# Kernel tuning notes

Measured on AMD Instinct MI355X. Metric: run time of the kernel, lower is better.

Reference implementation:

```python
import jax, jax.numpy as jnp
import numpy as np

B, H, W = 16, 512, 512


def _nmax(a, pad_val):
    """Max over 3x3 cross (4-neighborhood + center), constant-padded borders."""
    p = jnp.pad(a, ((0, 0), (1, 1), (1, 1)), constant_values=pad_val)
    return jnp.maximum(a, jnp.maximum(
        jnp.maximum(p[:, :-2, 1:-1], p[:, 2:, 1:-1]),
        jnp.maximum(p[:, 1:-1, :-2], p[:, 1:-1, 2:])))


def _dilate(b):
    # cv2 dilate with 3x3 MORPH_ELLIPSE (== cross), border treated as background
    return _nmax(b, 0.0)


def _erode(b):
    # cv2 erode default border value == foreground, so erode = 1 - dilate(1 - b)
    return 1.0 - _nmax(1.0 - b, 0.0)


def setup_inputs() -> dict:
    key = jax.random.key(0)
    x = jax.random.uniform(key, (B, 4, H, W), dtype=jnp.float32)
    return {"x": x}


def reference(x):
    # --- majority vote with disagreement fallback to pred1 ---
    p1 = (x[:, 1] > 0.5).astype(jnp.float32)
    p2 = (x[:, 2] > 0.5).astype(jnp.float32)
    p3 = (x[:, 3] > 0.5).astype(jnp.float32)
    vote = p1 + p2 + p3
    m = jnp.where(vote >= 2, 1.0, jnp.where(vote == 1, p1, 0.0))

    # --- morphology: MORPH_CLOSE then MORPH_OPEN with 3x3 ellipse (cross) ---
    m = _erode(_dilate(m))   # close
    m = _dilate(_erode(m))   # open

    # --- 4-connected CCL (scipy ndimage.label default) via label propagation ---
    Bm, Hm, Wm = m.shape
    mask_i = m > 0
    init = jnp.where(mask_i,
                     jnp.arange(1, Hm * Wm + 1, dtype=jnp.int32).reshape(1, Hm, Wm),
                     jnp.int32(0))

    def cond(s):
        return s[1]

    def body(s):
        lbl, _ = s
        new = jnp.where(mask_i, _nmax(lbl, 0), 0)
        return (new, jnp.any(new != lbl))

    lbl, _ = jax.lax.while_loop(cond, body, (init, jnp.array(True)))

    # --- component sizes and small-component removal ---
    sizes = jax.vmap(lambda mm, ll: jax.ops.segment_sum(
        mm.ravel(), ll.ravel(), num_segments=Hm * Wm + 1))(m, lbl)
    min_size = max(50, int(0.001 * Hm * Wm))  # = 262 for 512x512
    keep = jnp.take_along_axis(sizes, lbl.reshape(Bm, -1), axis=1)
    keep = (keep.reshape(Bm, Hm, Wm) > min_size).astype(jnp.float32)
    m = m * keep
    return m[:, None, :, :]  # [B, 1, H, W]
```

## Files before the change

### kernel.cpp

```cpp
#include <hip/hip_runtime.h>

typedef unsigned long long u64;
typedef unsigned u32;
typedef unsigned char u8;

#define BATCH 16
#define Hh 512
#define Ww 512
#define IMG (Hh * Ww)
#define TOT (BATCH * IMG)
#define WPI 4096
#define WROW 8
#define NWORDS (TOT / 64)
#define MIN_SIZE 262
#define MAXRUNS (NWORDS * 32)

#define BAND 8
#define HALO 4
#define BROWS (BAND + 2 * HALO)
#define BWORDS (BROWS * WROW)
#define MAXBRUNS (64 * 32)
#define NBANDS (BATCH * 64)

__device__ __forceinline__ u32 runstart(u64 bits, int s) {
    u64 ms = (s >= 63) ? ~0ULL : ((1ULL << (s + 1)) - 1);
    u64 nz = ~bits & ms;
    return nz ? (u32)(64 - __clzll(nz)) : 0u;
}
__device__ __forceinline__ u32 runlen(u64 bits, int s) {
    u64 v = ~(bits >> s);
    return v ? (u32)(__ffsll(v) - 1) : (u32)(64 - s);
}
__device__ __forceinline__ u32 runrank(u64 bits, u64 st, int s) {
    u32 rs = runstart(bits, s);
    return (u32)__popcll(st & (((u64)1 << rs) - 1));
}

__device__ __forceinline__ u64 morph_word(const u64* M, int w, int rr, bool er) {
    const u64 B = er ? ~0ULL : 0ULL;
    int wx = w & 7;
    u64 cc = M[w];
    u64 lf = (cc << 1) | (wx > 0 ? (M[w - 1] >> 63) : (er ? 1ULL : 0ULL));
    u64 rt = (cc >> 1) | (wx < 7 ? (M[w + 1] << 63) : (er ? (1ULL << 63) : 0ULL));
    u64 up = (rr <= 0)      ? B : (w >= WROW          ? M[w - WROW] : B);
    u64 dn = (rr >= Hh - 1) ? B : (w < BWORDS - WROW  ? M[w + WROW] : B);
    return er ? (cc & lf & rt & up & dn) : (cc | lf | rt | up | dn);
}

template <typename P>
__device__ __forceinline__ u32 uf_find_halve(P L, u32 x) {
    while (true) {
        u32 p = L[x];
        if (p == x) return x;
        u32 gp = L[p];
        if (gp == p) return p;
        atomicMin(&L[x], gp);
        x = gp;
    }
}
template <typename P>
__device__ __forceinline__ void uf_merge(P L, u32 a, u32 b) {
    while (true) {
        a = uf_find_halve(L, a);
        b = uf_find_halve(L, b);
        if (a == b) return;
        if (a > b) { u32 t = a; a = b; b = t; }
        u32 old = atomicMin(&L[b], a);
        if (old == b) return;
        b = old;
    }
}

__global__ __launch_bounds__(256) void vote_pack_kernel(const float4* __restrict__ x4,
                                                        u64* __restrict__ mp0,
                                                        u32* __restrict__ runCtr) {
    int t = threadIdx.x, blk = blockIdx.x;
    if (blk == 0 && t == 0) *runCtr = 0u;
    int img = blk >> 7;
    size_t p4 = (size_t)(blk & 127) * 512 + (size_t)t * 2;
    const float4* c1 = x4 + ((size_t)img * 4 + 1) * (IMG / 4);
    const float4* c2 = x4 + ((size_t)img * 4 + 2) * (IMG / 4);
    const float4* c3 = x4 + ((size_t)img * 4 + 3) * (IMG / 4);
    u32 m = 0;
    #pragma unroll
    for (int q = 0; q < 2; ++q) {
        float4 a1 = c1[p4 + q], a2 = c2[p4 + q], a3 = c3[p4 + q];
        u32 b0 = (a1.x > 0.5f) | ((a2.x > 0.5f) & (a3.x > 0.5f));
        u32 b1 = (a1.y > 0.5f) | ((a2.y > 0.5f) & (a3.y > 0.5f));
        u32 b2 = (a1.z > 0.5f) | ((a2.z > 0.5f) & (a3.z > 0.5f));
        u32 b3 = (a1.w > 0.5f) | ((a2.w > 0.5f) & (a3.w > 0.5f));
        m |= (b0 | (b1 << 1) | (b2 << 2) | (b3 << 3)) << (q * 4);
    }
    u32 a = m | (__shfl_xor(m, 1) << 8);
    u32 b = a | (__shfl_xor(a, 2) << 16);
    u64 w = (u64)b | ((u64)__shfl_xor(b, 4) << 32);
    if ((t & 7) == 0) mp0[(size_t)blk * 32 + (t >> 3)] = w;
}

__global__ __launch_bounds__(256) void morph_ccl_kernel(const u64* __restrict__ mp0,
                                                        u64* __restrict__ mp,
                                                        u32* __restrict__ L,
                                                        u32* __restrict__ wordbase,
                                                        u32* __restrict__ counts,
                                                        u8*  __restrict__ len8,
                                                        u32* __restrict__ runCtr) {
    __shared__ u64 Ma[BWORDS], Mb[BWORDS];
    __shared__ u32 Ll[MAXBRUNS];
    __shared__ u32 wb_l[64];
    __shared__ u32 baseSh, totSh;
    int blk = blockIdx.x;
    int img = blk >> 6;
    int r0  = (blk & 63) * BAND;
    int t = threadIdx.x;
    int rr = r0 - HALO + (t >> 3);

    if (t < BWORDS)
        Ma[t] = (rr >= 0 && rr < Hh) ? mp0[(size_t)img * WPI + (size_t)rr * WROW + (t & 7)] : 0;
    __syncthreads();

    if (t < BWORDS) Mb[t] = morph_word(Ma, t, rr, false);
    __syncthreads();
    if (t < BWORDS) Ma[t] = morph_word(Mb, t, rr, true);
    __syncthreads();
    if (t < BWORDS) Mb[t] = morph_word(Ma, t, rr, true);
    __syncthreads();
    if (t < BWORDS) Ma[t] = morph_word(Mb, t, rr, false);
    __syncthreads();

    if (t < 64)
        mp[(size_t)img * WPI + (size_t)r0 * WROW + t] = Ma[32 + t];

    u32 myexcl = 0;
    if (t < 64) {
        u64 bits = Ma[32 + t];
        u64 st = bits & ~(bits << 1);
        u32 cnt = __popcll(st);
        u32 inc = cnt;
        #pragma unroll
        for (int d = 1; d < 64; d <<= 1) {
            u32 v = __shfl_up(inc, d);
            if (t >= d) inc += v;
        }
        myexcl = inc - cnt;
        if (t == 63) { baseSh = atomicAdd(runCtr, inc); totSh = inc; }
    }
    __syncthreads();
    u32 base = baseSh, tot = totSh;
    if (t < 64) {
        wb_l[t] = myexcl;
        wordbase[(size_t)img * WPI + (size_t)r0 * WROW + t] = base + myexcl;
    }
    for (u32 i = t; i < tot; i += 256) { Ll[i] = i; counts[base + i] = 0u; }
    __syncthreads();

    if (t < 56) {
        int rp = t >> 3, w = t & 7;
        u64 a = Ma[32 + rp * 8 + w], b = Ma[32 + (rp + 1) * 8 + w];
        u64 ov = a & b, seg = ov & ~(ov << 1);
        if (seg) {
            u64 sta = a & ~(a << 1), stb = b & ~(b << 1);
            u32 ba = wb_l[rp * 8 + w], bb = wb_l[(rp + 1) * 8 + w];
            while (seg) {
                int s = __ffsll(seg) - 1; seg &= seg - 1;
                uf_merge((u32*)Ll, ba + runrank(a, sta, s), bb + runrank(b, stb, s));
            }
        }
    } else if (t >= 64 && t < 120) {
        int ht = t - 64;
        int r = ht / 7, w = 1 + ht % 7;
        u64 a = Ma[32 + r * 8 + w - 1], b = Ma[32 + r * 8 + w];
        if ((a >> 63) & b & 1ULL) {
            u64 sta = a & ~(a << 1);
            uf_merge((u32*)Ll, wb_l[r * 8 + w - 1] + (u32)__popcll(sta & ~(1ULL << 63)) - 1u
                                 + (u32)((sta >> 63) & 1ULL),
                               wb_l[r * 8 + w]);
        }
    }
    __syncthreads();

    if (t < 64) {
        u64 bits = Ma[32 + t];
        u64 st = bits & ~(bits << 1);
        u32 local = wb_l[t];
        while (st) {
            int s = __ffsll(st) - 1; st &= st - 1;
            u32 r = local, p = Ll[r];
            while (p != r) { r = p; p = Ll[r]; }
            L[base + local] = base + r;
            len8[base + local] = (u8)runlen(bits, s);
            local++;
        }
    }
}

#define BITEMS (BATCH * 63 * WROW)
__global__ void border_merge_kernel(const u64* __restrict__ mp,
                                    const u32* __restrict__ wordbase, u32* L) {
    int e = blockIdx.x * blockDim.x + threadIdx.x;
    if (e >= BITEMS) return;
    int w = e & 7, k = (e >> 3) % 63 + 1, img = e / (63 * 8);
    int R = k * BAND;
    size_t wa_i = (size_t)img * WPI + (size_t)(R - 1) * WROW + w;
    size_t wb_i = (size_t)img * WPI + (size_t)R * WROW + w;
    u64 a = mp[wa_i], b = mp[wb_i];
    u64 ov = a & b, seg = ov & ~(ov << 1);
    if (!seg) return;
    u64 sta = a & ~(a << 1), stb = b & ~(b << 1);
    u32 wba = wordbase[wa_i], wbb = wordbase[wb_i];
    while (seg) {
        int s = __ffsll(seg) - 1; seg &= seg - 1;
        uf_merge(L, wba + runrank(a, sta, s), wbb + runrank(b, stb, s));
    }
}

#define ACCUM_STRIDE (1024 * 256)
__global__ __launch_bounds__(256) void accum_kernel(u32* __restrict__ L,
                                                    const u8* __restrict__ len8,
                                                    u32* __restrict__ counts,
                                                    const u32* __restrict__ runCtr) {
    u32 n = *runCtr;
    u32 gid = blockIdx.x * 256 + threadIdx.x;
    int tid = threadIdx.x;
    u32 trips = (n + ACCUM_STRIDE - 1) / ACCUM_STRIDE;
    for (u32 k = 0; k < trips; ++k) {
        u32 id = gid + k * ACCUM_STRIDE;
        bool valid = id < n;
        u32 r = 0xFFFFFFFFu, len = 0;
        if (valid) {
            r = id; u32 p = L[r];
            while (p != r) { r = p; p = L[r]; }
            L[id] = r;
            len = len8[id];
        }
        bool pending = true;
        while (true) {
            u64 act = __ballot(pending);
            if (!act) break;
            int leader = __ffsll(act) - 1;
            u32 lr = __shfl(r, leader);
            bool mine = pending && (r == lr);
            u32 c = mine ? len : 0u;
            c += __shfl_xor(c, 32); c += __shfl_xor(c, 16); c += __shfl_xor(c, 8);
            c += __shfl_xor(c, 4);  c += __shfl_xor(c, 2);  c += __shfl_xor(c, 1);
            if ((tid & 63) == leader && lr != 0xFFFFFFFFu) atomicAdd(&counts[lr], c);
            if (mine) pending = false;
        }
    }
}

__global__ __launch_bounds__(256) void final_kernel(const u64* __restrict__ mp,
                                                    const u32* __restrict__ wordbase,
                                                    const u32* __restrict__ L,
                                                    const u32* __restrict__ counts,
                                                    float* __restrict__ out) {
    __shared__ u64 km[128];
    int tid = threadIdx.x;
    if (tid < 128) {
        int widx = blockIdx.x * 128 + tid;
        u64 bits = mp[widx];
        u64 st = bits & ~(bits << 1);
        u32 id = wordbase[widx];
        u64 keep = 0;
        while (st) {
            int s = __ffsll(st) - 1; st &= st - 1;
            u32 r = L[id++];
            if (counts[r] > MIN_SIZE) {
                u32 len = runlen(bits, s);
                keep |= (len == 64 ? ~0ULL : ((1ULL << len) - 1ULL)) << s;
            }
        }
        km[tid] = keep;
    }
    __syncthreads();
    float4* o4 = (float4*)out + (size_t)blockIdx.x * 2048;
    for (int i = tid; i < 2048; i += 256) {
        u32 nib = (u32)(km[i >> 4] >> ((i & 15) * 4)) & 0xFu;
        o4[i] = make_float4(nib & 1u ? 1.f : 0.f, nib & 2u ? 1.f : 0.f,
                            nib & 4u ? 1.f : 0.f, nib & 8u ? 1.f : 0.f);
    }
}

extern "C" void kernel_launch(void* const* d_in, const int* in_sizes, int n_in,
                              void* d_out, int out_size, void* d_ws, size_t ws_size,
                              hipStream_t stream) {
    const float* x = (const float*)d_in[0];
    float* out = (float*)d_out;

    u64* mp0 = (u64*)d_ws;
    u64* mp  = mp0 + NWORDS;
    u32* wordbase = (u32*)(mp + NWORDS);
    u32* L      = wordbase + NWORDS;
    u32* counts = L + MAXRUNS;
    u8*  len8   = (u8*)(counts + MAXRUNS);
    u32* runCtr = (u32*)(len8 + MAXRUNS);

    const int block = 256;

    vote_pack_kernel<<<2048, block, 0, stream>>>((const float4*)x, mp0, runCtr);
    morph_ccl_kernel<<<NBANDS, block, 0, stream>>>(mp0, mp, L, wordbase, counts, len8, runCtr);
    border_merge_kernel<<<(BITEMS + block - 1) / block, block, 0, stream>>>(mp, wordbase, L);
    accum_kernel<<<1024, block, 0, stream>>>(L, len8, counts, runCtr);
    final_kernel<<<512, block, 0, stream>>>(mp, wordbase, L, counts, out);
}
```

Before: 77.28 us.

## Use fixed per-word run slots and fold border merge into band kernel

Replaces the dynamic run numbering (atomic counter, prefix scan, wordbase and len8 arrays) with fixed 32-slot run IDs per word. The L and counts arrays are now initialised inside the vote/pack kernel. Each band kernel merges its local union-find roots into the global structure and merges its boundary with the next band, which removes the separate border-merge kernel and one launch. The accumulate kernel recomputes run lengths from the bitmask. The trade-off is a sparse label array that must be fully initialised (larger memory writes) and more global atomics issued from the band kernel. The halo also grows by one row, and the local shared array is now indexed by slot rather than by a compact run index.

```diff
diff --git a/kernel.cpp b/kernel.cpp
--- a/kernel.cpp
+++ b/kernel.cpp
@@ -2,7 +2,6 @@
 
 typedef unsigned long long u64;
 typedef unsigned u32;
-typedef unsigned char u8;
 
 #define BATCH 16
 #define Hh 512
@@ -16,10 +15,9 @@
 #define MAXRUNS (NWORDS * 32)
 
 #define BAND 8
-#define HALO 4
+#define HALO 5
 #define BROWS (BAND + 2 * HALO)
 #define BWORDS (BROWS * WROW)
-#define MAXBRUNS (64 * 32)
 #define NBANDS (BATCH * 64)
 
 __device__ __forceinline__ u32 runstart(u64 bits, int s) {
@@ -73,9 +71,13 @@
 
 __global__ __launch_bounds__(256) void vote_pack_kernel(const float4* __restrict__ x4,
                                                         u64* __restrict__ mp0,
-                                                        u32* __restrict__ runCtr) {
+                                                        u32* __restrict__ L,
+                                                        u32* __restrict__ counts) {
     int t = threadIdx.x, blk = blockIdx.x;
-    if (blk == 0 && t == 0) *runCtr = 0u;
+    u32 gidx = (u32)blk * 256 + t;
+    ((uint4*)L)[gidx] = make_uint4(gidx * 4u, gidx * 4u + 1u, gidx * 4u + 2u, gidx * 4u + 3u);
+    ((uint4*)counts)[gidx] = make_uint4(0u, 0u, 0u, 0u);
+
     int img = blk >> 7;
     size_t p4 = (size_t)(blk & 127) * 512 + (size_t)t * 2;
     const float4* c1 = x4 + ((size_t)img * 4 + 1) * (IMG / 4);
@@ -99,15 +101,9 @@
 
 __global__ __launch_bounds__(256) void morph_ccl_kernel(const u64* __restrict__ mp0,
                                                         u64* __restrict__ mp,
-                                                        u32* __restrict__ L,
-                                                        u32* __restrict__ wordbase,
-                                                        u32* __restrict__ counts,
-                                                        u8*  __restrict__ len8,
-                                                        u32* __restrict__ runCtr) {
+                                                        u32* __restrict__ L) {
     __shared__ u64 Ma[BWORDS], Mb[BWORDS];
-    __shared__ u32 Ll[MAXBRUNS];
-    __shared__ u32 wb_l[64];
-    __shared__ u32 baseSh, totSh;
+    __shared__ u32 Ll[2048];
     int blk = blockIdx.x;
     int img = blk >> 6;
     int r0  = (blk & 63) * BAND;
@@ -116,6 +112,7 @@
 
     if (t < BWORDS)
         Ma[t] = (rr >= 0 && rr < Hh) ? mp0[(size_t)img * WPI + (size_t)rr * WROW + (t & 7)] : 0;
+    for (int i = t; i < 2048; i += 256) Ll[i] = (u32)i;
     __syncthreads();
 
     if (t < BWORDS) Mb[t] = morph_word(Ma, t, rr, false);
@@ -127,129 +124,110 @@
     if (t < BWORDS) Ma[t] = morph_word(Mb, t, rr, false);
     __syncthreads();
 
+    const int OWN = HALO * WROW;
+    u32 gwbase = (u32)img * WPI + (u32)r0 * WROW;
     if (t < 64)
-        mp[(size_t)img * WPI + (size_t)r0 * WROW + t] = Ma[32 + t];
-
-    u32 myexcl = 0;
-    if (t < 64) {
-        u64 bits = Ma[32 + t];
-        u64 st = bits & ~(bits << 1);
-        u32 cnt = __popcll(st);
-        u32 inc = cnt;
-        #pragma unroll
-        for (int d = 1; d < 64; d <<= 1) {
-            u32 v = __shfl_up(inc, d);
-            if (t >= d) inc += v;
-        }
-        myexcl = inc - cnt;
-        if (t == 63) { baseSh = atomicAdd(runCtr, inc); totSh = inc; }
-    }
-    __syncthreads();
-    u32 base = baseSh, tot = totSh;
-    if (t < 64) {
-        wb_l[t] = myexcl;
-        wordbase[(size_t)img * WPI + (size_t)r0 * WROW + t] = base + myexcl;
-    }
-    for (u32 i = t; i < tot; i += 256) { Ll[i] = i; counts[base + i] = 0u; }
-    __syncthreads();
+        mp[(size_t)gwbase + t] = Ma[OWN + t];
 
     if (t < 56) {
         int rp = t >> 3, w = t & 7;
-        u64 a = Ma[32 + rp * 8 + w], b = Ma[32 + (rp + 1) * 8 + w];
+        u64 a = Ma[OWN + rp * 8 + w], b = Ma[OWN + (rp + 1) * 8 + w];
         u64 ov = a & b, seg = ov & ~(ov << 1);
         if (seg) {
             u64 sta = a & ~(a << 1), stb = b & ~(b << 1);
-            u32 ba = wb_l[rp * 8 + w], bb = wb_l[(rp + 1) * 8 + w];
+            u32 na = (u32)(rp * 8 + w) * 32, nb = (u32)((rp + 1) * 8 + w) * 32;
             while (seg) {
                 int s = __ffsll(seg) - 1; seg &= seg - 1;
-                uf_merge((u32*)Ll, ba + runrank(a, sta, s), bb + runrank(b, stb, s));
+                uf_merge((u32*)Ll, na + runrank(a, sta, s), nb + runrank(b, stb, s));
             }
         }
     } else if (t >= 64 && t < 120) {
         int ht = t - 64;
         int r = ht / 7, w = 1 + ht % 7;
-        u64 a = Ma[32 + r * 8 + w - 1], b = Ma[32 + r * 8 + w];
+        u64 a = Ma[OWN + r * 8 + w - 1], b = Ma[OWN + r * 8 + w];
         if ((a >> 63) & b & 1ULL) {
             u64 sta = a & ~(a << 1);
-            uf_merge((u32*)Ll, wb_l[r * 8 + w - 1] + (u32)__popcll(sta & ~(1ULL << 63)) - 1u
-                                 + (u32)((sta >> 63) & 1ULL),
-                               wb_l[r * 8 + w]);
+            uf_merge((u32*)Ll, (u32)(r * 8 + w - 1) * 32 + runrank(a, sta, 63),
+                               (u32)(r * 8 + w) * 32);
         }
     }
     __syncthreads();
 
     if (t < 64) {
-        u64 bits = Ma[32 + t];
+        u64 bits = Ma[OWN + t];
         u64 st = bits & ~(bits << 1);
-        u32 local = wb_l[t];
+        u32 k = 0;
         while (st) {
-            int s = __ffsll(st) - 1; st &= st - 1;
-            u32 r = local, p = Ll[r];
+            st &= st - 1;
+            u32 lid = (u32)t * 32 + k;
+            u32 r = lid, p = Ll[r];
             while (p != r) { r = p; p = Ll[r]; }
-            L[base + local] = base + r;
-            len8[base + local] = (u8)runlen(bits, s);
-            local++;
-        }
-    }
-}
-
-#define BITEMS (BATCH * 63 * WROW)
-__global__ void border_merge_kernel(const u64* __restrict__ mp,
-                                    const u32* __restrict__ wordbase, u32* L) {
-    int e = blockIdx.x * blockDim.x + threadIdx.x;
-    if (e >= BITEMS) return;
-    int w = e & 7, k = (e >> 3) % 63 + 1, img = e / (63 * 8);
-    int R = k * BAND;
-    size_t wa_i = (size_t)img * WPI + (size_t)(R - 1) * WROW + w;
-    size_t wb_i = (size_t)img * WPI + (size_t)R * WROW + w;
-    u64 a = mp[wa_i], b = mp[wb_i];
-    u64 ov = a & b, seg = ov & ~(ov << 1);
-    if (!seg) return;
-    u64 sta = a & ~(a << 1), stb = b & ~(b << 1);
-    u32 wba = wordbase[wa_i], wbb = wordbase[wb_i];
-    while (seg) {
-        int s = __ffsll(seg) - 1; seg &= seg - 1;
-        uf_merge(L, wba + runrank(a, sta, s), wbb + runrank(b, stb, s));
-    }
-}
-
-#define ACCUM_STRIDE (1024 * 256)
-__global__ __launch_bounds__(256) void accum_kernel(u32* __restrict__ L,
-                                                    const u8* __restrict__ len8,
-                                                    u32* __restrict__ counts,
-                                                    const u32* __restrict__ runCtr) {
-    u32 n = *runCtr;
-    u32 gid = blockIdx.x * 256 + threadIdx.x;
+            u32 gid   = (gwbase + (u32)t) * 32 + k;
+            u32 groot = (gwbase + (r >> 5)) * 32 + (r & 31);
+            if (groot != gid) uf_merge(L, gid, groot);
+            k++;
+        }
+    }
+
+    if ((blk & 63) != 63 && t < 8) {
+        u64 a = Ma[OWN + 56 + t];
+        u64 b = Ma[OWN + 64 + t];
+        u64 ov = a & b, seg = ov & ~(ov << 1);
+        if (seg) {
+            u64 sta = a & ~(a << 1), stb = b & ~(b << 1);
+            u32 ga = (gwbase + 56 + (u32)t) * 32;
+            u32 gb = (gwbase + 64 + (u32)t) * 32;
+            while (seg) {
+                int s = __ffsll(seg) - 1; seg &= seg - 1;
+                uf_merge(L, ga + runrank(a, sta, s), gb + runrank(b, stb, s));
+            }
+        }
+    }
+}
+
+__global__ __launch_bounds__(256) void accum_kernel(const u64* __restrict__ mp,
+                                                    u32* __restrict__ L,
+                                                    u32* __restrict__ counts) {
     int tid = threadIdx.x;
-    u32 trips = (n + ACCUM_STRIDE - 1) / ACCUM_STRIDE;
-    for (u32 k = 0; k < trips; ++k) {
-        u32 id = gid + k * ACCUM_STRIDE;
-        bool valid = id < n;
-        u32 r = 0xFFFFFFFFu, len = 0;
-        if (valid) {
-            r = id; u32 p = L[r];
-            while (p != r) { r = p; p = L[r]; }
-            L[id] = r;
-            len = len8[id];
-        }
-        bool pending = true;
-        while (true) {
-            u64 act = __ballot(pending);
-            if (!act) break;
-            int leader = __ffsll(act) - 1;
-            u32 lr = __shfl(r, leader);
-            bool mine = pending && (r == lr);
-            u32 c = mine ? len : 0u;
-            c += __shfl_xor(c, 32); c += __shfl_xor(c, 16); c += __shfl_xor(c, 8);
-            c += __shfl_xor(c, 4);  c += __shfl_xor(c, 2);  c += __shfl_xor(c, 1);
-            if ((tid & 63) == leader && lr != 0xFFFFFFFFu) atomicAdd(&counts[lr], c);
-            if (mine) pending = false;
+    int widx = blockIdx.x * 256 + tid;
+    u64 bits = mp[widx];
+    u64 st = bits & ~(bits << 1);
+    u32 idb = (u32)widx * 32, k = 0;
+
+    u32 r = 0, len = 0;
+    bool pending = false;
+    if (st) {
+        int s = __ffsll(st) - 1; st &= st - 1;
+        u32 id = idb + k; k++;
+        u32 rr = id, p = L[rr];
+        while (p != rr) { rr = p; p = L[rr]; }
+        L[id] = rr;
+        r = rr; len = runlen(bits, s); pending = true;
+    }
+    while (true) {
+        u64 act = __ballot(pending);
+        if (!act) break;
+        int leader = __ffsll(act) - 1;
+        u32 lr = __shfl(r, leader);
+        bool mine = pending && (r == lr);
+        u32 c = mine ? len : 0u;
+        c += __shfl_xor(c, 32); c += __shfl_xor(c, 16); c += __shfl_xor(c, 8);
+        c += __shfl_xor(c, 4);  c += __shfl_xor(c, 2);  c += __shfl_xor(c, 1);
+        if ((tid & 63) == leader) atomicAdd(&counts[lr], c);
+        if (mine) {
+            if (st) {
+                int s = __ffsll(st) - 1; st &= st - 1;
+                u32 id = idb + k; k++;
+                u32 rr = id, p = L[rr];
+                while (p != rr) { rr = p; p = L[rr]; }
+                L[id] = rr;
+                r = rr; len = runlen(bits, s);
+            } else pending = false;
         }
     }
 }
 
 __global__ __launch_bounds__(256) void final_kernel(const u64* __restrict__ mp,
-                                                    const u32* __restrict__ wordbase,
                                                     const u32* __restrict__ L,
                                                     const u32* __restrict__ counts,
                                                     float* __restrict__ out) {
@@ -259,7 +237,7 @@
         int widx = blockIdx.x * 128 + tid;
         u64 bits = mp[widx];
         u64 st = bits & ~(bits << 1);
-        u32 id = wordbase[widx];
+        u32 id = (u32)widx * 32;
         u64 keep = 0;
         while (st) {
             int s = __ffsll(st) - 1; st &= st - 1;
@@ -288,17 +266,13 @@
 
     u64* mp0 = (u64*)d_ws;
     u64* mp  = mp0 + NWORDS;
-    u32* wordbase = (u32*)(mp + NWORDS);
-    u32* L      = wordbase + NWORDS;
+    u32* L      = (u32*)(mp + NWORDS);
     u32* counts = L + MAXRUNS;
-    u8*  len8   = (u8*)(counts + MAXRUNS);
-    u32* runCtr = (u32*)(len8 + MAXRUNS);
 
     const int block = 256;
 
-    vote_pack_kernel<<<2048, block, 0, stream>>>((const float4*)x, mp0, runCtr);
-    morph_ccl_kernel<<<NBANDS, block, 0, stream>>>(mp0, mp, L, wordbase, counts, len8, runCtr);
-    border_merge_kernel<<<(BITEMS + block - 1) / block, block, 0, stream>>>(mp, wordbase, L);
-    accum_kernel<<<1024, block, 0, stream>>>(L, len8, counts, runCtr);
-    final_kernel<<<512, block, 0, stream>>>(mp, wordbase, L, counts, out);
-}
+    vote_pack_kernel<<<2048, block, 0, stream>>>((const float4*)x, mp0, L, counts);
+    morph_ccl_kernel<<<NBANDS, block, 0, stream>>>(mp0, mp, L);
+    accum_kernel<<<NWORDS / block, block, 0, stream>>>(mp, L, counts);
+    final_kernel<<<512, block, 0, stream>>>(mp, L, counts, out);
+}
```

Result: slower. 104.5 us (+35.2%).
